# Kernel optimization log

Hardware: AMD Instinct MI355X
Metric: run time of the kernel (lower is better)

Reference implementation:

```python
import jax, jax.numpy as jnp
import numpy as np

N, R, T = 40000, 2000, 500000   # node_size, rel_size, triple_size
D, DEPTH, PROXY_N = 128, 2, 64  # node_F, depth, proxy rows
DC = D * (DEPTH + 1)            # 384


def _unique_edges(rng, n_rows, n_cols, n_edges):
    # sorted, duplicate-free edge list -> matches torch.sparse coalesce() ordering
    keys = np.unique(rng.integers(0, n_rows * n_cols, size=int(n_edges * 1.05), dtype=np.int64))[:n_edges]
    assert keys.shape[0] == n_edges
    return np.stack([keys // n_cols, keys % n_cols], axis=1)


def _init_emb(key, r, c):
    w = jax.random.normal(key, (r, c), dtype=jnp.float32)
    return w / jnp.maximum(jnp.linalg.norm(w, axis=1, keepdims=True), 1e-12)


def setup_inputs() -> dict:
    rng = np.random.default_rng(0)
    adj = jnp.asarray(_unique_edges(rng, N, N, T))                    # [T,2] (src, dst)
    idx = jnp.stack([jnp.arange(T), jnp.asarray(rng.integers(0, R, T, dtype=np.int64))], axis=1)  # [T,2]
    val = jnp.ones((T,), jnp.float32)
    ent_m = jnp.asarray(_unique_edges(rng, N, N, T))
    rel_m = jnp.asarray(_unique_edges(rng, N, R, T))
    ks = jax.random.split(jax.random.key(0), 12)
    return {
        "ent_emb": _init_emb(ks[0], N, D),
        "rel_emb": _init_emb(ks[1], R, D),
        "e_gate": _init_emb(ks[2], DC, DC),
        "e_proxy": _init_emb(ks[3], PROXY_N, DC),
        "e_bias": _init_emb(ks[4], 1, DC),
        "e_attn": jnp.stack([_init_emb(ks[5], D, 1), _init_emb(ks[6], D, 1)]),
        "r_gate": _init_emb(ks[7], DC, DC),
        "r_proxy": _init_emb(ks[8], PROXY_N, DC),
        "r_bias": _init_emb(ks[9], 1, DC),
        "r_attn": jnp.stack([_init_emb(ks[10], D, 1), _init_emb(ks[11], D, 1)]),
        "val_input": val,
        "adj_input": adj,
        "index_input": idx,
        "ent_matrix": ent_m,
        "rel_matrix": rel_m,
    }


def _l2(x):
    return x / jnp.maximum(jnp.linalg.norm(x, axis=-1, keepdims=True), 1e-12)


def _seg_softmax(v, seg, n):
    m = jax.ops.segment_max(v, seg, num_segments=n)
    e = jnp.exp(v - m[seg])
    s = jax.ops.segment_sum(e, seg, num_segments=n)
    return e / s[seg]


def _adj_agg(edges, emb, n_rows):
    # torch.sparse.softmax over rows of an all-ones adjacency, then sparse @ emb
    rows, cols = edges[:, 0], edges[:, 1]
    w = _seg_softmax(jnp.zeros(edges.shape[0], emb.dtype), rows, n_rows)
    return jax.ops.segment_sum(w[:, None] * emb[cols], rows, num_segments=n_rows)


def _graph_attention(features, rel_emb, edges, sp_idx, sp_val, attn, gate_k, proxy, bias):
    n = features.shape[0]
    t = sp_val.shape[0]
    feats = jnp.tanh(features)
    outs = [feats]
    for l in range(DEPTH):
        # sparse (T,R) @ rel_emb -> per-edge relation embedding, then L2 normalize
        rels_sum = _l2(jax.ops.segment_sum(sp_val[:, None] * rel_emb[sp_idx[:, 1]], sp_idx[:, 0], num_segments=t))
        neighs = feats[edges[:, 1]]                                   # [T,D]
        neighs = neighs - 2.0 * jnp.sum(neighs * rels_sum, axis=1, keepdims=True) * rels_sum  # Householder reflection
        att = _seg_softmax((rels_sum @ attn[l])[:, 0], edges[:, 0], n)  # sparse row softmax
        feats = jnp.tanh(jax.ops.segment_sum(neighs * att[:, None], edges[:, 0], num_segments=n))
        outs.append(feats)
    outputs = jnp.concatenate(outs, axis=1)                           # [N, DC]
    pa = jax.nn.softmax(_l2(outputs) @ _l2(proxy).T, axis=-1)         # [N, 64]
    pf = outputs - pa @ proxy
    gate = jax.nn.sigmoid(pf @ gate_k + bias)
    return gate * outputs + (1.0 - gate) * pf


def reference(ent_emb, rel_emb, e_gate, e_proxy, e_bias, e_attn, r_gate, r_proxy, r_bias, r_attn, val_input, adj_input, index_input, ent_matrix, rel_matrix):
    ent_feature = _adj_agg(ent_matrix, ent_emb, N)                    # [N,D]
    rel_feature = _adj_agg(rel_matrix, rel_emb, N)                    # [N,D]
    out_e = _graph_attention(ent_feature, rel_emb, adj_input, index_input, val_input, e_attn, e_gate, e_proxy, e_bias)
    out_r = _graph_attention(rel_feature, rel_emb, adj_input, index_input, val_input, r_attn, r_gate, r_proxy, r_bias)
    # dropout_rate = 0.0 -> identity
    return jnp.concatenate([out_e, out_r], axis=-1)                   # [N, 2*DC]
```

## Files before the change

kernel.cpp:

```cpp
#include <hip/hip_runtime.h>
#include <hip/hip_fp16.h>


typedef __attribute__((ext_vector_type(8))) short bf16x8;
typedef __attribute__((ext_vector_type(4))) float f32x4;
typedef _Float16 h16x2 __attribute__((ext_vector_type(2)));
typedef unsigned short u16x8 __attribute__((ext_vector_type(8)));

__device__ __forceinline__ float wave_sum(float v) {
#pragma unroll
  for (int o = 32; o > 0; o >>= 1) v += __shfl_xor(v, o, 64);
  return v;
}
__device__ __forceinline__ float wave_max(float v) {
#pragma unroll
  for (int o = 32; o > 0; o >>= 1) v = fmaxf(v, __shfl_xor(v, o, 64));
  return v;
}
__device__ __forceinline__ unsigned short f2b(float x) {
  unsigned u = __builtin_bit_cast(unsigned, x);
  unsigned r = (u + 0x7fffu + ((u >> 16) & 1u)) >> 16;
  return (unsigned short)r;
}
__device__ __forceinline__ unsigned pkhalf2(float a, float b) {
  __half2 h = __floats2half2_rn(a, b);
  return __builtin_bit_cast(unsigned, h);
}
__device__ __forceinline__ float bcf(unsigned u) {
  return __builtin_bit_cast(float, u);
}
__device__ __forceinline__ float tanh_fast(float x) {
  float t = __expf(-2.f * fabsf(x));
  float y = (1.f - t) / (1.f + t);
  return copysignf(y, x);
}
__device__ __forceinline__ float fdot2u(unsigned a, unsigned b, float c) {
#if __has_builtin(__builtin_amdgcn_fdot2)
  return __builtin_amdgcn_fdot2(__builtin_bit_cast(h16x2, a),
                                __builtin_bit_cast(h16x2, b), c, false);
#else
  h16x2 x = __builtin_bit_cast(h16x2, a), y = __builtin_bit_cast(h16x2, b);
  return fmaf((float)x.x, (float)y.x, fmaf((float)x.y, (float)y.y, c));
#endif
}
__device__ __forceinline__ unsigned cvtpk_bf16(float lo, float hi) {
  unsigned r;
  asm("v_cvt_pk_bf16_f32 %0, %1, %2" : "=v"(r) : "v"(lo), "v"(hi));
  return r;
}
__device__ __forceinline__ bf16x8 h8_to_b8(uint4 u) {
  h16x2 h0 = __builtin_bit_cast(h16x2, u.x), h1 = __builtin_bit_cast(h16x2, u.y);
  h16x2 h2 = __builtin_bit_cast(h16x2, u.z), h3 = __builtin_bit_cast(h16x2, u.w);
  uint4 r;
  r.x = cvtpk_bf16((float)h0.x, (float)h0.y);
  r.y = cvtpk_bf16((float)h1.x, (float)h1.y);
  r.z = cvtpk_bf16((float)h2.x, (float)h2.y);
  r.w = cvtpk_bf16((float)h3.x, (float)h3.y);
  return __builtin_bit_cast(bf16x8, r);
}

__global__ void rowptr3_kernel(const int* __restrict__ e0,
                               const int* __restrict__ e1,
                               const int* __restrict__ e2, int T, int N,
                               int* __restrict__ p0, int* __restrict__ p1,
                               int* __restrict__ p2) {
  int tid = blockIdx.x * blockDim.x + threadIdx.x;
  int which = tid / (N + 1);
  int r = tid - which * (N + 1);
  if (which >= 3) return;
  const int* E = which == 0 ? e0 : (which == 1 ? e1 : e2);
  int* P = which == 0 ? p0 : (which == 1 ? p1 : p2);
  int lo = 0, hi = T;
  while (lo < hi) {
    int mid = (lo + hi) >> 1;
    if (E[2 * mid] < r) lo = mid + 1; else hi = mid;
  }
  P[r] = lo;
}

__global__ void relprep_kernel(const float* __restrict__ rel_emb,
                               const float* __restrict__ e_attn,
                               const float* __restrict__ r_attn, int R,
                               float* __restrict__ srel,
                               unsigned* __restrict__ rnorm,
                               unsigned* __restrict__ rel16) {
  int r = blockIdx.x * 4 + (threadIdx.x >> 6);
  int lane = threadIdx.x & 63;
  if (r >= R) return;
  float2 v  = *(const float2*)(rel_emb + (size_t)r * 128 + 2 * lane);
  float2 a0 = *(const float2*)(e_attn + 2 * lane);
  float2 a1 = *(const float2*)(e_attn + 128 + 2 * lane);
  float2 b0 = *(const float2*)(r_attn + 2 * lane);
  float2 b1 = *(const float2*)(r_attn + 128 + 2 * lane);
  float n  = wave_sum(v.x * v.x + v.y * v.y);
  float d0 = wave_sum(v.x * a0.x + v.y * a0.y);
  float d1 = wave_sum(v.x * a1.x + v.y * a1.y);
  float d2 = wave_sum(v.x * b0.x + v.y * b0.y);
  float d3 = wave_sum(v.x * b1.x + v.y * b1.y);
  float inv = 1.f / fmaxf(sqrtf(n), 1e-12f);
  rnorm[(size_t)r * 64 + lane] = pkhalf2(v.x * inv, v.y * inv);
  rel16[(size_t)r * 64 + lane] = pkhalf2(v.x, v.y);
  if (lane == 0) {
    srel[r]          = d0 * inv;
    srel[R + r]      = d1 * inv;
    srel[2 * R + r]  = d2 * inv;
    srel[3 * R + r]  = d3 * inv;
  }
}

__global__ void pack_f16_kernel(const float* __restrict__ src,
                                unsigned* __restrict__ dst, int n2) {
  int i = blockIdx.x * blockDim.x + threadIdx.x;
  if (i >= n2) return;
  float2 v = *(const float2*)(src + 2 * (size_t)i);
  dst[i] = pkhalf2(v.x, v.y);
}

__global__ __launch_bounds__(256) void stats_kernel(
    const int* __restrict__ ptr, const int* __restrict__ idx,
    const float* __restrict__ srel, int R, float* __restrict__ stats, int N) {
  int r = blockIdx.x * 4 + (threadIdx.x >> 6);
  if (r >= N) return;
  int lane = threadIdx.x & 63;
  int beg = ptr[r], end = ptr[r + 1];
  const float* s0 = srel;
  const float* s1 = srel + R;
  const float* s2 = srel + 2 * R;
  const float* s3 = srel + 3 * R;
  float m0 = -INFINITY, m1 = -INFINITY, m2 = -INFINITY, m3 = -INFINITY;
  for (int e = beg + lane; e < end; e += 64) {
    int rel = idx[2 * e + 1];
    m0 = fmaxf(m0, s0[rel]); m1 = fmaxf(m1, s1[rel]);
    m2 = fmaxf(m2, s2[rel]); m3 = fmaxf(m3, s3[rel]);
  }
#pragma unroll
  for (int o = 32; o > 0; o >>= 1) {
    m0 = fmaxf(m0, __shfl_xor(m0, o, 64));
    m1 = fmaxf(m1, __shfl_xor(m1, o, 64));
    m2 = fmaxf(m2, __shfl_xor(m2, o, 64));
    m3 = fmaxf(m3, __shfl_xor(m3, o, 64));
  }
  float d0 = 0.f, d1 = 0.f, d2 = 0.f, d3 = 0.f;
  for (int e = beg + lane; e < end; e += 64) {
    int rel = idx[2 * e + 1];
    d0 += __expf(s0[rel] - m0); d1 += __expf(s1[rel] - m1);
    d2 += __expf(s2[rel] - m2); d3 += __expf(s3[rel] - m3);
  }
#pragma unroll
  for (int o = 32; o > 0; o >>= 1) {
    d0 += __shfl_xor(d0, o, 64); d1 += __shfl_xor(d1, o, 64);
    d2 += __shfl_xor(d2, o, 64); d3 += __shfl_xor(d3, o, 64);
  }
  if (lane == 0) {
    float4 a, b;
    a.x = m0; a.y = (d0 > 0.f) ? 1.f / d0 : 0.f;
    a.z = m1; a.w = (d1 > 0.f) ? 1.f / d1 : 0.f;
    b.x = m2; b.y = (d2 > 0.f) ? 1.f / d2 : 0.f;
    b.z = m3; b.w = (d3 > 0.f) ? 1.f / d3 : 0.f;
    *(float4*)(stats + (size_t)r * 8) = a;
    *(float4*)(stats + (size_t)r * 8 + 4) = b;
  }
}

__global__ void weight_kernel(const int* __restrict__ adj,
                              const int* __restrict__ idx,
                              const float* __restrict__ srel, int R,
                              const float* __restrict__ stats,
                              unsigned* __restrict__ pk,
                              uint2* __restrict__ wt0,
                              uint2* __restrict__ wt1, int T) {
  int e = blockIdx.x * blockDim.x + threadIdx.x;
  if (e >= T) return;
  int row = adj[2 * e];
  int col = adj[2 * e + 1];
  int rel = idx[2 * e + 1];
  float4 a = *(const float4*)(stats + (size_t)row * 8);
  float4 b = *(const float4*)(stats + (size_t)row * 8 + 4);
  float w0 = __expf(srel[rel] - a.x) * a.y;
  float w1 = __expf(srel[R + rel] - a.z) * a.w;
  float w2 = __expf(srel[2 * R + rel] - b.x) * b.y;
  float w3 = __expf(srel[3 * R + rel] - b.z) * b.w;
  pk[e] = (unsigned)col | ((unsigned)rel << 16);
  wt0[e] = make_uint2(__builtin_bit_cast(unsigned, w0),
                      __builtin_bit_cast(unsigned, w2));
  wt1[e] = make_uint2(__builtin_bit_cast(unsigned, w1),
                      __builtin_bit_cast(unsigned, w3));
}

__global__ __launch_bounds__(256) void agg_fused_kernel(
    const int* __restrict__ ptrE, const int* __restrict__ edgesE,
    const unsigned* __restrict__ ent16, const int* __restrict__ ptrR,
    const int* __restrict__ edgesR, const unsigned* __restrict__ rel16,
    unsigned* __restrict__ fout, int N) {
  int r = blockIdx.x * 4 + (threadIdx.x >> 6);
  if (r >= N) return;
  int lane = threadIdx.x & 63;
  int g = lane >> 4, q = lane & 15;

  float aE[8] = {0, 0, 0, 0, 0, 0, 0, 0};
  float aR[8] = {0, 0, 0, 0, 0, 0, 0, 0};

  auto addh = [&](uint4 u, float* a) {
    h16x2 h0 = __builtin_bit_cast(h16x2, u.x), h1 = __builtin_bit_cast(h16x2, u.y);
    h16x2 h2 = __builtin_bit_cast(h16x2, u.z), h3 = __builtin_bit_cast(h16x2, u.w);
    a[0] = fmaf((float)h0.x, 1.f, a[0]); a[1] = fmaf((float)h0.y, 1.f, a[1]);
    a[2] = fmaf((float)h1.x, 1.f, a[2]); a[3] = fmaf((float)h1.y, 1.f, a[3]);
    a[4] = fmaf((float)h2.x, 1.f, a[4]); a[5] = fmaf((float)h2.y, 1.f, a[5]);
    a[6] = fmaf((float)h3.x, 1.f, a[6]); a[7] = fmaf((float)h3.y, 1.f, a[7]);
  };

  int begE = ptrE[r], endE = ptrE[r + 1];
  for (int e0 = begE; e0 < endE; e0 += 8) {
    int eA = e0 + g, eB = e0 + 4 + g;
    if (eA < endE)
      addh(*(const uint4*)(ent16 + (size_t)edgesE[2 * eA + 1] * 64 + 4 * q), aE);
    if (eB < endE)
      addh(*(const uint4*)(ent16 + (size_t)edgesE[2 * eB + 1] * 64 + 4 * q), aE);
  }
  int begR = ptrR[r], endR = ptrR[r + 1];
  for (int e0 = begR; e0 < endR; e0 += 8) {
    int eA = e0 + g, eB = e0 + 4 + g;
    if (eA < endR)
      addh(*(const uint4*)(rel16 + (size_t)edgesR[2 * eA + 1] * 64 + 4 * q), aR);
    if (eB < endR)
      addh(*(const uint4*)(rel16 + (size_t)edgesR[2 * eB + 1] * 64 + 4 * q), aR);
  }
#pragma unroll
  for (int j = 0; j < 8; ++j) {
    aE[j] += __shfl_xor(aE[j], 16, 64); aE[j] += __shfl_xor(aE[j], 32, 64);
    aR[j] += __shfl_xor(aR[j], 16, 64); aR[j] += __shfl_xor(aR[j], 32, 64);
  }
  float sE = (endE > begE) ? 1.f / (float)(endE - begE) : 0.f;
  float sR = (endR > begR) ? 1.f / (float)(endR - begR) : 0.f;
  if (g == 0) {
    float t[8];
#pragma unroll
    for (int j = 0; j < 8; ++j) t[j] = tanh_fast(aE[j] * sE);
    uint4 u;
    u.x = pkhalf2(t[0], t[1]); u.y = pkhalf2(t[2], t[3]);
    u.z = pkhalf2(t[4], t[5]); u.w = pkhalf2(t[6], t[7]);
    *(uint4*)(fout + (size_t)r * 128 + 4 * q) = u;
  } else if (g == 1) {
    float t[8];
#pragma unroll
    for (int j = 0; j < 8; ++j) t[j] = tanh_fast(aR[j] * sR);
    uint4 u;
    u.x = pkhalf2(t[0], t[1]); u.y = pkhalf2(t[2], t[3]);
    u.z = pkhalf2(t[4], t[5]); u.w = pkhalf2(t[6], t[7]);
    *(uint4*)(fout + (size_t)r * 128 + 64 + 4 * q) = u;
  }
}

__global__ __launch_bounds__(256) void layer_rec_kernel(
    const int* __restrict__ ptr, const unsigned* __restrict__ pk,
    const uint2* __restrict__ wt, const unsigned* __restrict__ rnorm,
    const unsigned* __restrict__ fin, unsigned* __restrict__ fout,
    int fstride, int N) {
  int r = blockIdx.x * 4 + (threadIdx.x >> 6);
  if (r >= N) return;
  int lane = threadIdx.x & 63;
  int g = lane >> 4, q = lane & 15;
  int beg = ptr[r], end = ptr[r + 1];

  float aE[8] = {0, 0, 0, 0, 0, 0, 0, 0};
  float aR[8] = {0, 0, 0, 0, 0, 0, 0, 0};

  auto accum = [&](uint4 F, uint4 V, float w, float s, float* a) {
    h16x2 f0 = __builtin_bit_cast(h16x2, F.x), v0 = __builtin_bit_cast(h16x2, V.x);
    h16x2 f1 = __builtin_bit_cast(h16x2, F.y), v1 = __builtin_bit_cast(h16x2, V.y);
    h16x2 f2 = __builtin_bit_cast(h16x2, F.z), v2 = __builtin_bit_cast(h16x2, V.z);
    h16x2 f3 = __builtin_bit_cast(h16x2, F.w), v3 = __builtin_bit_cast(h16x2, V.w);
    a[0] = fmaf((float)f0.x, w, fmaf((float)v0.x, s, a[0]));
    a[1] = fmaf((float)f0.y, w, fmaf((float)v0.y, s, a[1]));
    a[2] = fmaf((float)f1.x, w, fmaf((float)v1.x, s, a[2]));
    a[3] = fmaf((float)f1.y, w, fmaf((float)v1.y, s, a[3]));
    a[4] = fmaf((float)f2.x, w, fmaf((float)v2.x, s, a[4]));
    a[5] = fmaf((float)f2.y, w, fmaf((float)v2.y, s, a[5]));
    a[6] = fmaf((float)f3.x, w, fmaf((float)v3.x, s, a[6]));
    a[7] = fmaf((float)f3.y, w, fmaf((float)v3.y, s, a[7]));
  };

  for (int e0 = beg; e0 < end; e0 += 8) {
    int eA = e0 + g, eB = e0 + 4 + g;
    bool actA = eA < end, actB = eB < end;
    unsigned pkA = actA ? pk[eA] : 0u;
    unsigned pkB = actB ? pk[eB] : 0u;
    uint2 wA = actA ? wt[eA] : make_uint2(0u, 0u);
    uint2 wB = actB ? wt[eB] : make_uint2(0u, 0u);
    int colA = (int)(pkA & 0xFFFFu), relA = (int)(pkA >> 16);
    int colB = (int)(pkB & 0xFFFFu), relB = (int)(pkB >> 16);
    float wAE = bcf(wA.x), wAR = bcf(wA.y);
    float wBE = bcf(wB.x), wBR = bcf(wB.y);

    const unsigned* fA = fin + (size_t)colA * 128;
    const unsigned* fB = fin + (size_t)colB * 128;
    uint4 EA = *(const uint4*)(fA + 4 * q);
    uint4 RA = *(const uint4*)(fA + 64 + 4 * q);
    uint4 VA = *(const uint4*)(rnorm + (size_t)relA * 64 + 4 * q);
    uint4 EB = *(const uint4*)(fB + 4 * q);
    uint4 RB = *(const uint4*)(fB + 64 + 4 * q);
    uint4 VB = *(const uint4*)(rnorm + (size_t)relB * 64 + 4 * q);

    float dAE = fdot2u(EA.w, VA.w, fdot2u(EA.z, VA.z,
                fdot2u(EA.y, VA.y, fdot2u(EA.x, VA.x, 0.f))));
    float dAR = fdot2u(RA.w, VA.w, fdot2u(RA.z, VA.z,
                fdot2u(RA.y, VA.y, fdot2u(RA.x, VA.x, 0.f))));
    float dBE = fdot2u(EB.w, VB.w, fdot2u(EB.z, VB.z,
                fdot2u(EB.y, VB.y, fdot2u(EB.x, VB.x, 0.f))));
    float dBR = fdot2u(RB.w, VB.w, fdot2u(RB.z, VB.z,
                fdot2u(RB.y, VB.y, fdot2u(RB.x, VB.x, 0.f))));
#pragma unroll
    for (int m = 1; m < 16; m <<= 1) {
      dAE += __shfl_xor(dAE, m, 64);
      dAR += __shfl_xor(dAR, m, 64);
      dBE += __shfl_xor(dBE, m, 64);
      dBR += __shfl_xor(dBR, m, 64);
    }
    float sAE = -2.f * wAE * dAE, sAR = -2.f * wAR * dAR;
    float sBE = -2.f * wBE * dBE, sBR = -2.f * wBR * dBR;
    accum(EA, VA, wAE, sAE, aE);
    accum(RA, VA, wAR, sAR, aR);
    accum(EB, VB, wBE, sBE, aE);
    accum(RB, VB, wBR, sBR, aR);
  }

#pragma unroll
  for (int j = 0; j < 8; ++j) {
    aE[j] += __shfl_xor(aE[j], 16, 64); aE[j] += __shfl_xor(aE[j], 32, 64);
    aR[j] += __shfl_xor(aR[j], 16, 64); aR[j] += __shfl_xor(aR[j], 32, 64);
  }
  if (g == 0) {
    float t[8];
#pragma unroll
    for (int j = 0; j < 8; ++j) t[j] = tanh_fast(aE[j]);
    uint4 u;
    u.x = pkhalf2(t[0], t[1]); u.y = pkhalf2(t[2], t[3]);
    u.z = pkhalf2(t[4], t[5]); u.w = pkhalf2(t[6], t[7]);
    *(uint4*)(fout + (size_t)r * fstride + 4 * q) = u;
  } else if (g == 1) {
    float t[8];
#pragma unroll
    for (int j = 0; j < 8; ++j) t[j] = tanh_fast(aR[j]);
    uint4 u;
    u.x = pkhalf2(t[0], t[1]); u.y = pkhalf2(t[2], t[3]);
    u.z = pkhalf2(t[4], t[5]); u.w = pkhalf2(t[6], t[7]);
    *(uint4*)(fout + (size_t)r * fstride + 64 + 4 * q) = u;
  }
}

__device__ __forceinline__ void pack_one(const float* __restrict__ src,
                                         unsigned short* __restrict__ dst,
                                         int NT, int srcld, int mode, int f,
                                         int lane) {
  int kt = f / NT, nt = f % NT;
  int kbase = 32 * kt + 8 * (lane >> 4);
  int n = 16 * nt + (lane & 15);
  unsigned short tmp[8];
#pragma unroll
  for (int j = 0; j < 8; ++j) {
    int k = kbase + j;
    float v = (mode == 0) ? src[(size_t)k * srcld + n] : src[(size_t)n * srcld + k];
    tmp[j] = f2b(v);
  }
  *(bf16x8*)(dst + ((size_t)f * 64 + lane) * 8) = *(bf16x8*)tmp;
}
__global__ void pack_all_kernel(const float* eP, const float* eG,
                                const float* rP, const float* rG,
                                unsigned short* b1e, unsigned short* b2e,
                                unsigned short* b3e, unsigned short* b1r,
                                unsigned short* b2r, unsigned short* b3r) {
  int f = blockIdx.x * 4 + (threadIdx.x >> 6);
  int lane = threadIdx.x & 63;
  if (f < 48)       pack_one(eP, b1e, 4, 384, 1, f, lane);
  else if (f < 96)  pack_one(eP, b2e, 24, 384, 0, f - 48, lane);
  else if (f < 384) pack_one(eG, b3e, 24, 384, 0, f - 96, lane);
  else if (f < 432) pack_one(rP, b1r, 4, 384, 1, f - 384, lane);
  else if (f < 480) pack_one(rP, b2r, 24, 384, 0, f - 432, lane);
  else if (f < 768) pack_one(rG, b3r, 24, 384, 0, f - 480, lane);
}

__global__ __launch_bounds__(512) void final_v3_kernel(
    const unsigned* __restrict__ f0, const unsigned* __restrict__ f1,
    const unsigned* __restrict__ f2, int s2, int plane,
    const unsigned short* __restrict__ B1, const unsigned short* __restrict__ B2,
    const unsigned short* __restrict__ B3, const float* __restrict__ bias,
    float* __restrict__ gout, int coloff) {
  __shared__ __align__(16) unsigned sOutH[32][204];
  __shared__ __align__(16) unsigned sUraw[32][204];
  __shared__ __align__(16) unsigned short sPaB[32][72];
  __shared__ float sInv[32];
  unsigned short* sOutHs = (unsigned short*)&sOutH[0][0];
  unsigned short* sPfs = (unsigned short*)&sUraw[0][0];
  float (*sPa)[68] = (float(*)[68]) & sUraw[0][0];

  const int t = threadIdx.x;
  const int w = t >> 6, lane = t & 63;
  const int lr = lane & 15, lg = lane >> 4;
  const int row0 = blockIdx.x * 32;

  for (int i = t; i < 32 * 48; i += 512) {
    int r = i / 48, c4 = i % 48;
    int buf = c4 >> 4, j = c4 & 15;
    const unsigned* src;
    if (buf == 0)      src = f0 + (size_t)(row0 + r) * 128 + plane + 4 * j;
    else if (buf == 1) src = f1 + (size_t)(row0 + r) * 128 + plane + 4 * j;
    else               src = f2 + (size_t)(row0 + r) * s2 + plane + 4 * j;
    *(uint4*)&sOutH[r][c4 * 4] = *(const uint4*)src;
  }
  __syncthreads();

  for (int rr = 4 * w; rr < 4 * w + 4; ++rr) {
    float s = 0.f;
#pragma unroll
    for (int k = 0; k < 3; ++k) {
      unsigned u = sOutH[rr][3 * lane + k];
      s = fdot2u(u, u, s);
    }
    s = wave_sum(s);
    if (lane == 0) sInv[rr] = 1.f / fmaxf(sqrtf(s), 1e-12f);
  }
  __syncthreads();

  {
    int rt = w >> 2, ct = w & 3;
    f32x4 acc = {0.f, 0.f, 0.f, 0.f};
#pragma unroll
    for (int kt = 0; kt < 12; ++kt) {
      bf16x8 a = h8_to_b8(*(const uint4*)&sOutH[rt * 16 + lr][16 * kt + 4 * lg]);
      bf16x8 b = *(const bf16x8*)(B1 + ((size_t)(kt * 4 + ct) * 64 + lane) * 8);
      acc = __builtin_amdgcn_mfma_f32_16x16x32_bf16(a, b, acc, 0, 0, 0);
    }
#pragma unroll
    for (int rr = 0; rr < 4; ++rr) {
      int row = rt * 16 + 4 * lg + rr;
      sPa[row][ct * 16 + lr] = acc[rr] * sInv[row];
    }
  }
  __syncthreads();

  for (int rr = 4 * w; rr < 4 * w + 4; ++rr) {
    float v = sPa[rr][lane];
    float mx = wave_max(v);
    float e = __expf(v - mx);
    float s = wave_sum(e);
    sPaB[rr][lane] = f2b(e / s);
  }
  __syncthreads();

  {
    int rt = w >> 2, ntb = (w & 3) * 6;
    bf16x8 a0 = *(const bf16x8*)&sPaB[rt * 16 + lr][8 * lg];
    bf16x8 a1 = *(const bf16x8*)&sPaB[rt * 16 + lr][32 + 8 * lg];
#pragma unroll
    for (int i = 0; i < 6; ++i) {
      int nt = ntb + i;
      f32x4 acc = {0.f, 0.f, 0.f, 0.f};
      bf16x8 b0 = *(const bf16x8*)(B2 + ((size_t)nt * 64 + lane) * 8);
      bf16x8 b1 = *(const bf16x8*)(B2 + ((size_t)(24 + nt) * 64 + lane) * 8);
      acc = __builtin_amdgcn_mfma_f32_16x16x32_bf16(a0, b0, acc, 0, 0, 0);
      acc = __builtin_amdgcn_mfma_f32_16x16x32_bf16(a1, b1, acc, 0, 0, 0);
#pragma unroll
      for (int rr = 0; rr < 4; ++rr) {
        int row = rt * 16 + 4 * lg + rr, col = 16 * nt + lr;
        float outv = (float)__builtin_bit_cast(_Float16, sOutHs[row * 408 + col]);
        float pf = outv - acc[rr];
        sPfs[row * 408 + col] = __builtin_bit_cast(unsigned short, (_Float16)pf);
      }
    }
  }
  __syncthreads();

  {
    int rt = w >> 2, ntb = (w & 3) * 6;
    bf16x8 a3[12];
#pragma unroll
    for (int kt = 0; kt < 12; ++kt)
      a3[kt] = h8_to_b8(*(const uint4*)&sUraw[rt * 16 + lr][16 * kt + 4 * lg]);
#pragma unroll
    for (int i = 0; i < 6; ++i) {
      int nt = ntb + i;
      f32x4 acc = {0.f, 0.f, 0.f, 0.f};
#pragma unroll
      for (int kt = 0; kt < 12; ++kt) {
        bf16x8 b = *(const bf16x8*)(B3 + ((size_t)(kt * 24 + nt) * 64 + lane) * 8);
        acc = __builtin_amdgcn_mfma_f32_16x16x32_bf16(a3[kt], b, acc, 0, 0, 0);
      }
      float bv = bias[16 * nt + lr];
#pragma unroll
      for (int rr = 0; rr < 4; ++rr) {
        int row = rt * 16 + 4 * lg + rr, col = 16 * nt + lr;
        float g = 1.f / (1.f + __expf(-(acc[rr] + bv)));
        float outv = (float)__builtin_bit_cast(_Float16, sOutHs[row * 408 + col]);
        float pfv = (float)__builtin_bit_cast(_Float16, sPfs[row * 408 + col]);
        gout[(size_t)(row0 + row) * 768 + coloff + col] =
            g * outv + (1.f - g) * pfv;
      }
    }
  }
}

extern "C" void kernel_launch(void* const* d_in, const int* in_sizes, int n_in,
                              void* d_out, int out_size, void* d_ws,
                              size_t ws_size, hipStream_t stream) {
  (void)n_in; (void)out_size; (void)ws_size;
  const float* ent_emb = (const float*)d_in[0];
  const float* rel_emb = (const float*)d_in[1];
  const float* e_gate  = (const float*)d_in[2];
  const float* e_proxy = (const float*)d_in[3];
  const float* e_bias  = (const float*)d_in[4];
  const float* e_attn  = (const float*)d_in[5];
  const float* r_gate  = (const float*)d_in[6];
  const float* r_proxy = (const float*)d_in[7];
  const float* r_bias  = (const float*)d_in[8];
  const float* r_attn  = (const float*)d_in[9];
  const int* adj   = (const int*)d_in[11];
  const int* idx   = (const int*)d_in[12];
  const int* ent_m = (const int*)d_in[13];
  const int* rel_m = (const int*)d_in[14];
  const int N = in_sizes[0] / 128;
  const int R = in_sizes[1] / 128;
  const int T = in_sizes[10];
  float* out = (float*)d_out;

  char* w = (char*)d_ws;
  size_t used = 0;
  auto alloc = [&](size_t bytes) {
    void* p = (void*)(w + used);
    used += (bytes + 255) & ~(size_t)255;
    return p;
  };
  int* ptr_adj  = (int*)alloc((size_t)(N + 1) * sizeof(int));
  int* ptr_ent  = (int*)alloc((size_t)(N + 1) * sizeof(int));
  int* ptr_rel  = (int*)alloc((size_t)(N + 1) * sizeof(int));
  float* srel   = (float*)alloc((size_t)4 * R * sizeof(float));
  unsigned short* b1e = (unsigned short*)alloc(48 * 1024);
  unsigned short* b2e = (unsigned short*)alloc(48 * 1024);
  unsigned short* b3e = (unsigned short*)alloc(288 * 1024);
  unsigned short* b1r = (unsigned short*)alloc(48 * 1024);
  unsigned short* b2r = (unsigned short*)alloc(48 * 1024);
  unsigned short* b3r = (unsigned short*)alloc(288 * 1024);
  unsigned* rnorm = (unsigned*)alloc((size_t)R * 64 * 4);
  unsigned* rel16 = (unsigned*)alloc((size_t)R * 64 * 4);
  unsigned* ent16 = (unsigned*)alloc((size_t)N * 64 * 4);
  unsigned* fsrc0 = (unsigned*)alloc((size_t)N * 128 * 4);
  unsigned* fsrc1 = (unsigned*)alloc((size_t)N * 128 * 4);
  float* stats = (float*)alloc((size_t)N * 8 * sizeof(float));
  unsigned* pk = (unsigned*)alloc((size_t)T * 4);
  uint2* wt0 = (uint2*)alloc((size_t)T * 8);
  uint2* wt1 = (uint2*)alloc((size_t)T * 8);

  dim3 b256(256);
  rowptr3_kernel<<<(3 * (N + 1) + 255) / 256, b256, 0, stream>>>(
      adj, ent_m, rel_m, T, N, ptr_adj, ptr_ent, ptr_rel);
  relprep_kernel<<<(R + 3) / 4, b256, 0, stream>>>(rel_emb, e_attn, r_attn, R,
                                                   srel, rnorm, rel16);
  pack_f16_kernel<<<(N * 64 + 255) / 256, b256, 0, stream>>>(ent_emb, ent16,
                                                             N * 64);
  pack_all_kernel<<<192, b256, 0, stream>>>(e_proxy, e_gate, r_proxy, r_gate,
                                            b1e, b2e, b3e, b1r, b2r, b3r);

  int grow = (N + 3) / 4;
  stats_kernel<<<grow, b256, 0, stream>>>(ptr_adj, idx, srel, R, stats, N);
  weight_kernel<<<(T + 255) / 256, b256, 0, stream>>>(adj, idx, srel, R, stats,
                                                      pk, wt0, wt1, T);
  agg_fused_kernel<<<grow, b256, 0, stream>>>(ptr_ent, ent_m, ent16, ptr_rel,
                                              rel_m, rel16, fsrc0, N);
  unsigned* gscratch = (unsigned*)out + 512;
  layer_rec_kernel<<<grow, b256, 0, stream>>>(ptr_adj, pk, wt0, rnorm, fsrc0,
                                              fsrc1, 128, N);
  layer_rec_kernel<<<grow, b256, 0, stream>>>(ptr_adj, pk, wt1, rnorm, fsrc1,
                                              gscratch, 768, N);

  int fblocks = (N + 31) / 32;
  final_v3_kernel<<<fblocks, dim3(512), 0, stream>>>(
      fsrc0, fsrc1, gscratch, 768, 0, b1e, b2e, b3e, e_bias, out, 0);
  final_v3_kernel<<<fblocks, dim3(512), 0, stream>>>(
      fsrc0, fsrc1, gscratch, 768, 64, b1r, b2r, b3r, r_bias, out, 384);
}
```

Baseline: 341.6 us.

## Switch final kernel to 32x32 f16 MFMA with 64-row tiles

The final proxy/gate kernel now uses 32x32x16 f16 MFMA instead of 16x16x32 bf16. This removes the fp16-to-bf16 conversion of the A operands, and each block handles 64 rows instead of 32. The weight packing switches to fp16 in the matching 32-wide fragment layout. The pf values are written in place into the output tile so the second shared buffer is no longer needed, and outputs are kept in registers. Larger tiles raise register and LDS pressure, and the proxy GEMM runs on only 4 of the 8 waves.

```diff
diff --git a/kernel.cpp b/kernel.cpp
--- a/kernel.cpp
+++ b/kernel.cpp
@@ -2,10 +2,10 @@
 #include <hip/hip_fp16.h>
 
 
-typedef __attribute__((ext_vector_type(8))) short bf16x8;
 typedef __attribute__((ext_vector_type(4))) float f32x4;
 typedef _Float16 h16x2 __attribute__((ext_vector_type(2)));
-typedef unsigned short u16x8 __attribute__((ext_vector_type(8)));
+typedef _Float16 f16x8 __attribute__((ext_vector_type(8)));
+typedef float f32x16 __attribute__((ext_vector_type(16)));
 
 __device__ __forceinline__ float wave_sum(float v) {
 #pragma unroll
@@ -16,11 +16,6 @@
 #pragma unroll
   for (int o = 32; o > 0; o >>= 1) v = fmaxf(v, __shfl_xor(v, o, 64));
   return v;
-}
-__device__ __forceinline__ unsigned short f2b(float x) {
-  unsigned u = __builtin_bit_cast(unsigned, x);
-  unsigned r = (u + 0x7fffu + ((u >> 16) & 1u)) >> 16;
-  return (unsigned short)r;
 }
 __device__ __forceinline__ unsigned pkhalf2(float a, float b) {
   __half2 h = __floats2half2_rn(a, b);
@@ -28,6 +23,12 @@
 }
 __device__ __forceinline__ float bcf(unsigned u) {
   return __builtin_bit_cast(float, u);
+}
+__device__ __forceinline__ unsigned short f2h(float x) {
+  return __builtin_bit_cast(unsigned short, (_Float16)x);
+}
+__device__ __forceinline__ float h2f(unsigned short h) {
+  return (float)__builtin_bit_cast(_Float16, h);
 }
 __device__ __forceinline__ float tanh_fast(float x) {
   float t = __expf(-2.f * fabsf(x));
@@ -42,21 +43,6 @@
   h16x2 x = __builtin_bit_cast(h16x2, a), y = __builtin_bit_cast(h16x2, b);
   return fmaf((float)x.x, (float)y.x, fmaf((float)x.y, (float)y.y, c));
 #endif
-}
-__device__ __forceinline__ unsigned cvtpk_bf16(float lo, float hi) {
-  unsigned r;
-  asm("v_cvt_pk_bf16_f32 %0, %1, %2" : "=v"(r) : "v"(lo), "v"(hi));
-  return r;
-}
-__device__ __forceinline__ bf16x8 h8_to_b8(uint4 u) {
-  h16x2 h0 = __builtin_bit_cast(h16x2, u.x), h1 = __builtin_bit_cast(h16x2, u.y);
-  h16x2 h2 = __builtin_bit_cast(h16x2, u.z), h3 = __builtin_bit_cast(h16x2, u.w);
-  uint4 r;
-  r.x = cvtpk_bf16((float)h0.x, (float)h0.y);
-  r.y = cvtpk_bf16((float)h1.x, (float)h1.y);
-  r.z = cvtpk_bf16((float)h2.x, (float)h2.y);
-  r.w = cvtpk_bf16((float)h3.x, (float)h3.y);
-  return __builtin_bit_cast(bf16x8, r);
 }
 
 __global__ void rowptr3_kernel(const int* __restrict__ e0,
@@ -203,10 +189,10 @@
   auto addh = [&](uint4 u, float* a) {
     h16x2 h0 = __builtin_bit_cast(h16x2, u.x), h1 = __builtin_bit_cast(h16x2, u.y);
     h16x2 h2 = __builtin_bit_cast(h16x2, u.z), h3 = __builtin_bit_cast(h16x2, u.w);
-    a[0] = fmaf((float)h0.x, 1.f, a[0]); a[1] = fmaf((float)h0.y, 1.f, a[1]);
-    a[2] = fmaf((float)h1.x, 1.f, a[2]); a[3] = fmaf((float)h1.y, 1.f, a[3]);
-    a[4] = fmaf((float)h2.x, 1.f, a[4]); a[5] = fmaf((float)h2.y, 1.f, a[5]);
-    a[6] = fmaf((float)h3.x, 1.f, a[6]); a[7] = fmaf((float)h3.y, 1.f, a[7]);
+    a[0] += (float)h0.x; a[1] += (float)h0.y;
+    a[2] += (float)h1.x; a[3] += (float)h1.y;
+    a[4] += (float)h2.x; a[5] += (float)h2.y;
+    a[6] += (float)h3.x; a[7] += (float)h3.y;
   };
 
   int begE = ptrE[r], endE = ptrE[r + 1];
@@ -348,21 +334,21 @@
   }
 }
 
-__device__ __forceinline__ void pack_one(const float* __restrict__ src,
-                                         unsigned short* __restrict__ dst,
-                                         int NT, int srcld, int mode, int f,
-                                         int lane) {
+__device__ __forceinline__ void pack_one32(const float* __restrict__ src,
+                                           unsigned short* __restrict__ dst,
+                                           int NT, int srcld, int mode, int f,
+                                           int lane) {
   int kt = f / NT, nt = f % NT;
-  int kbase = 32 * kt + 8 * (lane >> 4);
-  int n = 16 * nt + (lane & 15);
+  int kbase = 16 * kt + 8 * (lane >> 5);
+  int n = 32 * nt + (lane & 31);
   unsigned short tmp[8];
 #pragma unroll
   for (int j = 0; j < 8; ++j) {
     int k = kbase + j;
     float v = (mode == 0) ? src[(size_t)k * srcld + n] : src[(size_t)n * srcld + k];
-    tmp[j] = f2b(v);
-  }
-  *(bf16x8*)(dst + ((size_t)f * 64 + lane) * 8) = *(bf16x8*)tmp;
+    tmp[j] = f2h(v);
+  }
+  *(uint4*)(dst + ((size_t)f * 64 + lane) * 8) = *(uint4*)tmp;
 }
 __global__ void pack_all_kernel(const float* eP, const float* eG,
                                 const float* rP, const float* rG,
@@ -371,34 +357,32 @@
                                 unsigned short* b2r, unsigned short* b3r) {
   int f = blockIdx.x * 4 + (threadIdx.x >> 6);
   int lane = threadIdx.x & 63;
-  if (f < 48)       pack_one(eP, b1e, 4, 384, 1, f, lane);
-  else if (f < 96)  pack_one(eP, b2e, 24, 384, 0, f - 48, lane);
-  else if (f < 384) pack_one(eG, b3e, 24, 384, 0, f - 96, lane);
-  else if (f < 432) pack_one(rP, b1r, 4, 384, 1, f - 384, lane);
-  else if (f < 480) pack_one(rP, b2r, 24, 384, 0, f - 432, lane);
-  else if (f < 768) pack_one(rG, b3r, 24, 384, 0, f - 480, lane);
-}
-
-__global__ __launch_bounds__(512) void final_v3_kernel(
+  if (f < 48)       pack_one32(eP, b1e, 2, 384, 1, f, lane);
+  else if (f < 96)  pack_one32(eP, b2e, 12, 384, 0, f - 48, lane);
+  else if (f < 384) pack_one32(eG, b3e, 12, 384, 0, f - 96, lane);
+  else if (f < 432) pack_one32(rP, b1r, 2, 384, 1, f - 384, lane);
+  else if (f < 480) pack_one32(rP, b2r, 12, 384, 0, f - 432, lane);
+  else if (f < 768) pack_one32(rG, b3r, 12, 384, 0, f - 480, lane);
+}
+
+__global__ __launch_bounds__(512) void final_v4_kernel(
     const unsigned* __restrict__ f0, const unsigned* __restrict__ f1,
     const unsigned* __restrict__ f2, int s2, int plane,
     const unsigned short* __restrict__ B1, const unsigned short* __restrict__ B2,
     const unsigned short* __restrict__ B3, const float* __restrict__ bias,
     float* __restrict__ gout, int coloff) {
-  __shared__ __align__(16) unsigned sOutH[32][204];
-  __shared__ __align__(16) unsigned sUraw[32][204];
-  __shared__ __align__(16) unsigned short sPaB[32][72];
-  __shared__ float sInv[32];
+  __shared__ __align__(16) unsigned sOutH[64][204];
+  __shared__ __align__(16) float sPa[64][68];
+  __shared__ __align__(16) unsigned short sPaH[64][72];
+  __shared__ float sInv[64];
   unsigned short* sOutHs = (unsigned short*)&sOutH[0][0];
-  unsigned short* sPfs = (unsigned short*)&sUraw[0][0];
-  float (*sPa)[68] = (float(*)[68]) & sUraw[0][0];
 
   const int t = threadIdx.x;
   const int w = t >> 6, lane = t & 63;
-  const int lr = lane & 15, lg = lane >> 4;
-  const int row0 = blockIdx.x * 32;
-
-  for (int i = t; i < 32 * 48; i += 512) {
+  const int l31 = lane & 31, l5 = lane >> 5;
+  const int row0 = blockIdx.x * 64;
+
+  for (int i = t; i < 64 * 48; i += 512) {
     int r = i / 48, c4 = i % 48;
     int buf = c4 >> 4, j = c4 & 15;
     const unsigned* src;
@@ -409,7 +393,7 @@
   }
   __syncthreads();
 
-  for (int rr = 4 * w; rr < 4 * w + 4; ++rr) {
+  for (int rr = 8 * w; rr < 8 * w + 8; ++rr) {
     float s = 0.f;
 #pragma unroll
     for (int k = 0; k < 3; ++k) {
@@ -421,80 +405,103 @@
   }
   __syncthreads();
 
-  {
-    int rt = w >> 2, ct = w & 3;
-    f32x4 acc = {0.f, 0.f, 0.f, 0.f};
-#pragma unroll
-    for (int kt = 0; kt < 12; ++kt) {
-      bf16x8 a = h8_to_b8(*(const uint4*)&sOutH[rt * 16 + lr][16 * kt + 4 * lg]);
-      bf16x8 b = *(const bf16x8*)(B1 + ((size_t)(kt * 4 + ct) * 64 + lane) * 8);
-      acc = __builtin_amdgcn_mfma_f32_16x16x32_bf16(a, b, acc, 0, 0, 0);
-    }
-#pragma unroll
-    for (int rr = 0; rr < 4; ++rr) {
-      int row = rt * 16 + 4 * lg + rr;
-      sPa[row][ct * 16 + lr] = acc[rr] * sInv[row];
+  if (w < 4) {
+    int rt = w >> 1, ct = w & 1;
+    f32x16 acc = {0.f, 0.f, 0.f, 0.f, 0.f, 0.f, 0.f, 0.f,
+                  0.f, 0.f, 0.f, 0.f, 0.f, 0.f, 0.f, 0.f};
+#pragma unroll
+    for (int kt = 0; kt < 24; ++kt) {
+      f16x8 a = __builtin_bit_cast(
+          f16x8, *(const uint4*)&sOutH[rt * 32 + l31][8 * kt + 4 * l5]);
+      f16x8 b = *(const f16x8*)(B1 + ((size_t)(kt * 2 + ct) * 64 + lane) * 8);
+      acc = __builtin_amdgcn_mfma_f32_32x32x16_f16(a, b, acc, 0, 0, 0);
+    }
+#pragma unroll
+    for (int reg = 0; reg < 16; ++reg) {
+      int row = rt * 32 + (reg & 3) + 8 * (reg >> 2) + 4 * l5;
+      sPa[row][ct * 32 + l31] = acc[reg] * sInv[row];
     }
   }
   __syncthreads();
 
-  for (int rr = 4 * w; rr < 4 * w + 4; ++rr) {
+  for (int rr = 8 * w; rr < 8 * w + 8; ++rr) {
     float v = sPa[rr][lane];
     float mx = wave_max(v);
     float e = __expf(v - mx);
     float s = wave_sum(e);
-    sPaB[rr][lane] = f2b(e / s);
+    sPaH[rr][lane] = f2h(e / s);
   }
   __syncthreads();
 
+  const int rt = w & 1, ntb = 3 * (w >> 1);
+  unsigned outv[3][8];
   {
-    int rt = w >> 2, ntb = (w & 3) * 6;
-    bf16x8 a0 = *(const bf16x8*)&sPaB[rt * 16 + lr][8 * lg];
-    bf16x8 a1 = *(const bf16x8*)&sPaB[rt * 16 + lr][32 + 8 * lg];
-#pragma unroll
-    for (int i = 0; i < 6; ++i) {
-      int nt = ntb + i;
-      f32x4 acc = {0.f, 0.f, 0.f, 0.f};
-      bf16x8 b0 = *(const bf16x8*)(B2 + ((size_t)nt * 64 + lane) * 8);
-      bf16x8 b1 = *(const bf16x8*)(B2 + ((size_t)(24 + nt) * 64 + lane) * 8);
-      acc = __builtin_amdgcn_mfma_f32_16x16x32_bf16(a0, b0, acc, 0, 0, 0);
-      acc = __builtin_amdgcn_mfma_f32_16x16x32_bf16(a1, b1, acc, 0, 0, 0);
-#pragma unroll
-      for (int rr = 0; rr < 4; ++rr) {
-        int row = rt * 16 + 4 * lg + rr, col = 16 * nt + lr;
-        float outv = (float)__builtin_bit_cast(_Float16, sOutHs[row * 408 + col]);
-        float pf = outv - acc[rr];
-        sPfs[row * 408 + col] = __builtin_bit_cast(unsigned short, (_Float16)pf);
+    f32x16 acc2[3];
+#pragma unroll
+    for (int s = 0; s < 3; ++s)
+#pragma unroll
+      for (int i = 0; i < 16; ++i) acc2[s][i] = 0.f;
+#pragma unroll
+    for (int kt = 0; kt < 4; ++kt) {
+      f16x8 a = __builtin_bit_cast(
+          f16x8, *(const uint4*)&sPaH[rt * 32 + l31][16 * kt + 8 * l5]);
+#pragma unroll
+      for (int s = 0; s < 3; ++s) {
+        f16x8 b = *(const f16x8*)(B2 + ((size_t)(kt * 12 + ntb + s) * 64 + lane) * 8);
+        acc2[s] = __builtin_amdgcn_mfma_f32_32x32x16_f16(a, b, acc2[s], 0, 0, 0);
       }
     }
+#pragma unroll
+    for (int s = 0; s < 3; ++s) {
+      int col = 32 * (ntb + s) + l31;
+#pragma unroll
+      for (int p = 0; p < 8; ++p) {
+        int ra = rt * 32 + ((2 * p) & 3) + 8 * (p >> 1) + 4 * l5;
+        unsigned short u0 = sOutHs[ra * 408 + col];
+        unsigned short u1 = sOutHs[(ra + 1) * 408 + col];
+        outv[s][p] = (unsigned)u0 | ((unsigned)u1 << 16);
+        float pf0 = h2f(u0) - acc2[s][2 * p];
+        float pf1 = h2f(u1) - acc2[s][2 * p + 1];
+        sOutHs[ra * 408 + col] = f2h(pf0);
+        sOutHs[(ra + 1) * 408 + col] = f2h(pf1);
+      }
+    }
   }
   __syncthreads();
 
-  {
-    int rt = w >> 2, ntb = (w & 3) * 6;
-    bf16x8 a3[12];
-#pragma unroll
-    for (int kt = 0; kt < 12; ++kt)
-      a3[kt] = h8_to_b8(*(const uint4*)&sUraw[rt * 16 + lr][16 * kt + 4 * lg]);
-#pragma unroll
-    for (int i = 0; i < 6; ++i) {
-      int nt = ntb + i;
-      f32x4 acc = {0.f, 0.f, 0.f, 0.f};
-#pragma unroll
-      for (int kt = 0; kt < 12; ++kt) {
-        bf16x8 b = *(const bf16x8*)(B3 + ((size_t)(kt * 24 + nt) * 64 + lane) * 8);
-        acc = __builtin_amdgcn_mfma_f32_16x16x32_bf16(a3[kt], b, acc, 0, 0, 0);
-      }
-      float bv = bias[16 * nt + lr];
-#pragma unroll
-      for (int rr = 0; rr < 4; ++rr) {
-        int row = rt * 16 + 4 * lg + rr, col = 16 * nt + lr;
-        float g = 1.f / (1.f + __expf(-(acc[rr] + bv)));
-        float outv = (float)__builtin_bit_cast(_Float16, sOutHs[row * 408 + col]);
-        float pfv = (float)__builtin_bit_cast(_Float16, sPfs[row * 408 + col]);
-        gout[(size_t)(row0 + row) * 768 + coloff + col] =
-            g * outv + (1.f - g) * pfv;
-      }
+  f32x16 acc3[3];
+#pragma unroll
+  for (int s = 0; s < 3; ++s)
+#pragma unroll
+    for (int i = 0; i < 16; ++i) acc3[s][i] = 0.f;
+#pragma unroll
+  for (int kt = 0; kt < 24; ++kt) {
+    f16x8 a = __builtin_bit_cast(
+        f16x8, *(const uint4*)&sOutH[rt * 32 + l31][8 * kt + 4 * l5]);
+#pragma unroll
+    for (int s = 0; s < 3; ++s) {
+      f16x8 b = *(const f16x8*)(B3 + ((size_t)(kt * 12 + ntb + s) * 64 + lane) * 8);
+      acc3[s] = __builtin_amdgcn_mfma_f32_32x32x16_f16(a, b, acc3[s], 0, 0, 0);
+    }
+  }
+
+#pragma unroll
+  for (int s = 0; s < 3; ++s) {
+    int col = 32 * (ntb + s) + l31;
+    float bv = bias[col];
+#pragma unroll
+    for (int p = 0; p < 8; ++p) {
+      int ra = rt * 32 + ((2 * p) & 3) + 8 * (p >> 1) + 4 * l5;
+      float g0 = 1.f / (1.f + __expf(-(acc3[s][2 * p] + bv)));
+      float g1 = 1.f / (1.f + __expf(-(acc3[s][2 * p + 1] + bv)));
+      float pf0 = h2f(sOutHs[ra * 408 + col]);
+      float pf1 = h2f(sOutHs[(ra + 1) * 408 + col]);
+      unsigned ov = outv[s][p];
+      float o0 = h2f((unsigned short)(ov & 0xffffu));
+      float o1 = h2f((unsigned short)(ov >> 16));
+      gout[(size_t)(row0 + ra) * 768 + coloff + col] = g0 * o0 + (1.f - g0) * pf0;
+      gout[(size_t)(row0 + ra + 1) * 768 + coloff + col] =
+          g1 * o1 + (1.f - g1) * pf1;
     }
   }
 }
@@ -571,9 +578,9 @@
   layer_rec_kernel<<<grow, b256, 0, stream>>>(ptr_adj, pk, wt1, rnorm, fsrc1,
                                               gscratch, 768, N);
 
-  int fblocks = (N + 31) / 32;
-  final_v3_kernel<<<fblocks, dim3(512), 0, stream>>>(
+  int fblocks = (N + 63) / 64;
+  final_v4_kernel<<<fblocks, dim3(512), 0, stream>>>(
       fsrc0, fsrc1, gscratch, 768, 0, b1e, b2e, b3e, e_bias, out, 0);
-  final_v3_kernel<<<fblocks, dim3(512), 0, stream>>>(
+  final_v4_kernel<<<fblocks, dim3(512), 0, stream>>>(
       fsrc0, fsrc1, gscratch, 768, 64, b1r, b2r, b3r, r_bias, out, 384);
 }
```

Measured after the change: 351.6 us. +2.9%, slower.
